# Performance work log

Hardware: AMD Instinct MI355X
Metric: run time of the kernel (lower is better)

## Reference

```python
import jax, jax.numpy as jnp
import numpy as np

DIM = 128


def setup_inputs() -> dict:
    key = jax.random.key(0)
    k1, k2, k3, k4 = jax.random.split(key, 4)
    x = jax.random.normal(k1, (8, 32768, DIM), dtype=jnp.float32)
    # nn.Linear(dim, dim*3, bias=False): weight applied as x @ W.T; store as [dim, 3*dim]
    W_qkv = jax.random.normal(k2, (DIM, 3 * DIM), dtype=jnp.float32) * (DIM ** -0.5)
    W_out = jax.random.normal(k3, (DIM, DIM), dtype=jnp.float32) * (DIM ** -0.5)
    b_out = jax.random.normal(k4, (DIM,), dtype=jnp.float32) * 0.01
    return {"x": x, "W_qkv": W_qkv, "W_out": W_out, "b_out": b_out}


def reference(x, W_qkv, W_out, b_out):
    dim = x.shape[-1]
    scale = dim ** -0.5
    qkv = x @ W_qkv  # [b, n, 3d]
    q, k, v = jnp.split(qkv, 3, axis=-1)
    q = jax.nn.softmax(q, axis=-1) * scale
    k = jax.nn.softmax(k, axis=-1)
    v = jax.nn.softmax(v, axis=-1)
    context = jnp.einsum('bnd,bne->bde', q, k)  # [b, d, d]
    out = jnp.einsum('bde,bne->bnd', context, v)  # [b, n, d]
    return out @ W_out + b_out
```

## Files before the change

### kernel.cpp

```cpp
#include <hip/hip_runtime.h>

#define SEQ 32768
#define QSCALE 0.08838834764831845f
#define NCH 16

typedef __attribute__((ext_vector_type(8))) short short8;
typedef __attribute__((ext_vector_type(8))) __bf16 bf16x8;
typedef __attribute__((ext_vector_type(16))) float f32x16;
typedef __attribute__((ext_vector_type(4))) float f32x4;
typedef __attribute__((ext_vector_type(4))) int int4v;
typedef __attribute__((ext_vector_type(2))) int int2v;

#define SWZ(r, c) ((((r) << 7) + (c)) ^ (((r) & 15) << 3))
#define PSWZ(ch, n) ((((ch) << 6) + (n)) ^ (((ch) & 7) << 3))

__device__ __forceinline__ int cvtpk(float lo, float hi) {
  int r;
  asm("v_cvt_pk_bf16_f32 %0, %1, %2" : "=v"(r) : "v"(lo), "v"(hi));
  return r;
}

__device__ __forceinline__ short bf16b(float f) {
  unsigned u = __builtin_bit_cast(unsigned, f);
  u += 0x7fffu + ((u >> 16) & 1u);
  return (short)(u >> 16);
}

__device__ __forceinline__ f32x16 mfma_ii(int4v a, int4v b, f32x16 c) {
  return __builtin_amdgcn_mfma_f32_32x32x16_bf16(
      __builtin_bit_cast(bf16x8, a), __builtin_bit_cast(bf16x8, b), c, 0, 0, 0);
}

__device__ __forceinline__ int4v build_frag(float e0, float e1, float e2, float e3,
                                            float e4, float e5, float e6, float e7,
                                            int hi) {
  int t0 = cvtpk(e0, e1), t1 = cvtpk(e2, e3);
  int t2 = cvtpk(e4, e5), t3 = cvtpk(e6, e7);
  const int u0 = __shfl_xor(t2, 32), u1 = __shfl_xor(t3, 32);
  const int u2 = __shfl_xor(t0, 32), u3 = __shfl_xor(t1, 32);
  int4v f;
  f[0] = hi ? u0 : t0;
  f[1] = hi ? u1 : t1;
  f[2] = hi ? t2 : u2;
  f[3] = hi ? t3 : u3;
  return f;
}

__global__ void la_prep(const float* __restrict__ Wqkv, int4v* __restrict__ Wf) {
  const int fid = blockIdx.x * 256 + threadIdx.x;
  if (fid >= 6144) return;
  const int side = fid >> 11;
  const int rem = fid & 2047;
  const int tile = rem >> 9;
  const int ks = (rem >> 6) & 7;
  const int lane = rem & 63;
  const int k0 = ks * 16 + ((lane >> 5) << 3);
  const int col = side * 128 + tile * 32 + (lane & 31);
  int4v f;
  #pragma unroll
  for (int a = 0; a < 4; ++a)
    f[a] = cvtpk(Wqkv[(k0 + 2 * a) * 384 + col], Wqkv[(k0 + 2 * a + 1) * 384 + col]);
  Wf[fid] = f;
}

__global__ __launch_bounds__(1024, 4)
void la_pass1(const float* __restrict__ x, const int4v* __restrict__ Wf,
              float* __restrict__ partials) {
  __shared__ __align__(16) short xs[2][64 * 128];
  __shared__ __align__(16) short ptile[2][2][128 * 64];
  __shared__ __align__(16) float sumbuf[2][2][2][32][4];

  const int tid = threadIdx.x;
  const int lane = tid & 63;
  const int wv = tid >> 6;
  const int l31 = lane & 31;
  const int hi = lane >> 5;
  const int koff = hi << 3;
  const int h = wv >> 3;
  const int c = (wv >> 1) & 3;
  const int rh = wv & 1;
  const int td = wv >> 2;
  const int te = wv & 3;
  const int b = blockIdx.x >> 5;
  const int strip = blockIdx.x & 31;
  const long base = (long)b * SEQ + (long)strip * (NCH * 64);

  int4v wf[8];
  #pragma unroll
  for (int ks = 0; ks < 8; ++ks)
    wf[ks] = Wf[((((h << 2) + c) << 3) + ks) * 64 + lane];

  const int lr = tid >> 4;
  const int cf = (tid & 15) << 3;
  {
    const float* xp = x + (base + lr) * 128 + cf;
    f32x4 u0 = *(const f32x4*)xp;
    f32x4 u1 = *(const f32x4*)(xp + 4);
    int4v p;
    p[0] = cvtpk(u0[0], u0[1]); p[1] = cvtpk(u0[2], u0[3]);
    p[2] = cvtpk(u1[0], u1[1]); p[3] = cvtpk(u1[2], u1[3]);
    *(int4v*)&xs[0][SWZ(lr, cf)] = p;
  }
  __syncthreads();

  f32x16 ctx = {0.f};
  const int r0 = rh << 5;
  for (int i = 0; i < NCH; ++i) {
    const int cur = i & 1;
    const int inx = (i + 1 < NCH) ? i + 1 : i;
    const float* xp = x + (base + inx * 64 + lr) * 128 + cf;
    f32x4 u0 = *(const f32x4*)xp;
    f32x4 u1 = *(const f32x4*)(xp + 4);

    f32x16 acc = {0.f};
    #pragma unroll
    for (int ks = 0; ks < 8; ++ks) {
      const int4v xf = *(const int4v*)&xs[cur][SWZ(r0 + l31, (ks << 4) + koff)];
      acc = mfma_ii(wf[ks], xf, acc);
    }
    {
      float sa = 0.f, sb = 0.f;
      #pragma unroll
      for (int r = 0; r < 16; r += 2) {
        acc[r] = __expf(acc[r]);     sa += acc[r];
        acc[r + 1] = __expf(acc[r + 1]); sb += acc[r + 1];
      }
      float s = sa + sb;
      s += __shfl_xor(s, 32);
      if (!hi) sumbuf[cur][h][rh][l31][c] = s;
    }

    {
      int4v p;
      p[0] = cvtpk(u0[0], u0[1]); p[1] = cvtpk(u0[2], u0[3]);
      p[2] = cvtpk(u1[0], u1[1]); p[3] = cvtpk(u1[2], u1[3]);
      *(int4v*)&xs[cur ^ 1][SWZ(lr, cf)] = p;
    }
    __syncthreads();

    if (i > 0) {
      const int pb = cur ^ 1;
      #pragma unroll
      for (int ks = 0; ks < 4; ++ks) {
        const int4v aq = *(const int4v*)&ptile[pb][0][PSWZ((td << 5) + l31, (ks << 4) + koff)];
        const int4v bk = *(const int4v*)&ptile[pb][1][PSWZ((te << 5) + l31, (ks << 4) + koff)];
        ctx = mfma_ii(aq, bk, ctx);
      }
    }

    {
      short* pt = &ptile[cur][h][0];
      const int n = (rh << 5) + l31;
      if (h == 0) {
        const f32x4 sq = *(const f32x4*)&sumbuf[cur][0][rh][l31][0];
        const f32x4 sk = *(const f32x4*)&sumbuf[cur][1][rh][l31][0];
        const float invn = QSCALE * __builtin_amdgcn_rcpf(
            (sq[0] + sq[1] + sq[2] + sq[3]) * (sk[0] + sk[1] + sk[2] + sk[3]));
        #pragma unroll
        for (int r = 0; r < 16; ++r) {
          const int ch = (c << 5) + (r & 3) + ((r >> 2) << 3) + (hi << 2);
          pt[PSWZ(ch, n)] = bf16b(acc[r] * invn);
        }
      } else {
        #pragma unroll
        for (int r = 0; r < 16; ++r) {
          const int ch = (c << 5) + (r & 3) + ((r >> 2) << 3) + (hi << 2);
          pt[PSWZ(ch, n)] = bf16b(acc[r]);
        }
      }
    }
  }
  __syncthreads();
  {
    const int pb = (NCH - 1) & 1;
    #pragma unroll
    for (int ks = 0; ks < 4; ++ks) {
      const int4v aq = *(const int4v*)&ptile[pb][0][PSWZ((td << 5) + l31, (ks << 4) + koff)];
      const int4v bk = *(const int4v*)&ptile[pb][1][PSWZ((te << 5) + l31, (ks << 4) + koff)];
      ctx = mfma_ii(aq, bk, ctx);
    }
  }

  float* pout = partials + (long)blockIdx.x * 16384;
  #pragma unroll
  for (int r = 0; r < 16; ++r) {
    const int drow = (td << 5) + (r & 3) + ((r >> 2) << 3) + (hi << 2);
    pout[(drow << 7) + (te << 5) + l31] = ctx[r];
  }
}

__global__ void la_reduce(const float* __restrict__ partials, float* __restrict__ ctx,
                          int strips) {
  const int b = blockIdx.x >> 4;
  const int sl = blockIdx.x & 15;
  const int idx = (sl << 10) + ((int)threadIdx.x << 2);
  f32x4 acc = {0.f};
  for (int st = 0; st < strips; ++st)
    acc += *(const f32x4*)(partials + ((long)(b * strips + st) << 14) + idx);
  *(f32x4*)(ctx + ((long)b << 14) + idx) = acc;
}

__global__ void la_mkern(const float* __restrict__ ctx, const float* __restrict__ Wout,
                         int4v* __restrict__ Mtf) {
  __shared__ __align__(16) float cl[128 * 132];
  __shared__ float wo[128 * 32];
  const int tid = threadIdx.x;
  const int b = blockIdx.x >> 2;
  const int d0 = (blockIdx.x & 3) << 5;
  const float* cp = ctx + ((long)b << 14);
  for (int i = tid << 2; i < 16384; i += 1024) {
    f32x4 v = *(const f32x4*)(cp + i);
    *(f32x4*)&cl[(i >> 7) * 132 + (i & 127)] = v;
  }
  for (int i = tid; i < 128 * 32; i += 256)
    wo[i] = Wout[((i >> 5) << 7) + d0 + (i & 31)];
  __syncthreads();
  const int dq = tid >> 3;
  const int e0 = (tid & 7) << 4;
  float acc[16];
  #pragma unroll
  for (int i = 0; i < 16; ++i) acc[i] = 0.0f;
  for (int d = 0; d < 128; ++d) {
    const float w = wo[(d << 5) + dq];
    const float* cr = &cl[d * 132 + e0];
    #pragma unroll
    for (int i = 0; i < 16; ++i) acc[i] += cr[i] * w;
  }
  const int dp = d0 + dq;
  const int j = dp & 3, l = dp >> 2, ks = e0 >> 4;
  int4v lo, hi2;
  lo[0] = cvtpk(acc[0], acc[1]);   lo[1] = cvtpk(acc[2], acc[3]);
  lo[2] = cvtpk(acc[4], acc[5]);   lo[3] = cvtpk(acc[6], acc[7]);
  hi2[0] = cvtpk(acc[8], acc[9]);  hi2[1] = cvtpk(acc[10], acc[11]);
  hi2[2] = cvtpk(acc[12], acc[13]); hi2[3] = cvtpk(acc[14], acc[15]);
  int4v* dst = Mtf + ((((long)b << 2) + j) * 8 + ks) * 64;
  dst[l] = lo;
  dst[32 + l] = hi2;
}

__global__ __launch_bounds__(256, 3)
void la_pass2(const float* __restrict__ x, const int4v* __restrict__ Wf,
              const int4v* __restrict__ Mtf, const float* __restrict__ bout,
              float* __restrict__ out) {
  __shared__ __align__(16) short xs[4][32 * 128];

  const int tid = threadIdx.x;
  const int lane = tid & 63;
  const int wv = tid >> 6;
  const int l31 = lane & 31;
  const int hi = lane >> 5;
  const int koff = hi << 3;
  const int b = blockIdx.x >> 8;
  const int chunk = blockIdx.x & 255;
  const long row0 = (long)b * SEQ + (long)chunk * 128 + (wv << 5);

  {
    const float* xb = x + row0 * 128;
    f32x4 u[16];
    #pragma unroll
    for (int t = 0; t < 16; ++t)
      u[t] = *(const f32x4*)(xb + t * 256 + lane * 4);
    #pragma unroll
    for (int t = 0; t < 16; ++t) {
      const int flat = t * 256 + lane * 4;
      int2v w;
      w[0] = cvtpk(u[t][0], u[t][1]);
      w[1] = cvtpk(u[t][2], u[t][3]);
      *(int2v*)&xs[wv][SWZ(flat >> 7, flat & 127)] = w;
    }
  }
  const f32x4 bias = *(const f32x4*)(bout + (l31 << 2));
  asm volatile("s_waitcnt lgkmcnt(0)" ::: "memory");
  __builtin_amdgcn_sched_barrier(0);

  int4v xfr[8];
  #pragma unroll
  for (int ks = 0; ks < 8; ++ks)
    xfr[ks] = *(const int4v*)&xs[wv][SWZ(l31, (ks << 4) + koff)];

  const int4v* WvT = Wf + 2 * 2048;
  f32x16 a0 = {0.f}, a1 = {0.f}, a2 = {0.f}, a3 = {0.f};
  #pragma unroll
  for (int ks = 0; ks < 8; ++ks) {
    a0 = mfma_ii(WvT[(0 * 8 + ks) * 64 + lane], xfr[ks], a0);
    a1 = mfma_ii(WvT[(1 * 8 + ks) * 64 + lane], xfr[ks], a1);
    a2 = mfma_ii(WvT[(2 * 8 + ks) * 64 + lane], xfr[ks], a2);
    a3 = mfma_ii(WvT[(3 * 8 + ks) * 64 + lane], xfr[ks], a3);
  }

  float s = 0.f;
  #pragma unroll
  for (int r = 0; r < 16; ++r) {
    a0[r] = __expf(a0[r]); s += a0[r];
    a1[r] = __expf(a1[r]); s += a1[r];
    a2[r] = __expf(a2[r]); s += a2[r];
    a3[r] = __expf(a3[r]); s += a3[r];
  }
  s += __shfl_xor(s, 32);
  const float inv = __builtin_amdgcn_rcpf(s);
  #pragma unroll
  for (int r = 0; r < 16; ++r) {
    a0[r] *= inv; a1[r] *= inv; a2[r] *= inv; a3[r] *= inv;
  }

  int4v vf[8];
  vf[0] = build_frag(a0[0], a0[1], a0[2], a0[3], a0[4], a0[5], a0[6], a0[7], hi);
  vf[1] = build_frag(a0[8], a0[9], a0[10], a0[11], a0[12], a0[13], a0[14], a0[15], hi);
  vf[2] = build_frag(a1[0], a1[1], a1[2], a1[3], a1[4], a1[5], a1[6], a1[7], hi);
  vf[3] = build_frag(a1[8], a1[9], a1[10], a1[11], a1[12], a1[13], a1[14], a1[15], hi);
  vf[4] = build_frag(a2[0], a2[1], a2[2], a2[3], a2[4], a2[5], a2[6], a2[7], hi);
  vf[5] = build_frag(a2[8], a2[9], a2[10], a2[11], a2[12], a2[13], a2[14], a2[15], hi);
  vf[6] = build_frag(a3[0], a3[1], a3[2], a3[3], a3[4], a3[5], a3[6], a3[7], hi);
  vf[7] = build_frag(a3[8], a3[9], a3[10], a3[11], a3[12], a3[13], a3[14], a3[15], hi);

  const int4v* MtB = Mtf + ((long)b << 11);
  f32x16 o0 = {0.f}, o1 = {0.f}, o2 = {0.f}, o3 = {0.f};
  #pragma unroll
  for (int ks = 0; ks < 8; ++ks) {
    o0 = mfma_ii(vf[ks], MtB[(0 * 8 + ks) * 64 + lane], o0);
    o1 = mfma_ii(vf[ks], MtB[(1 * 8 + ks) * 64 + lane], o1);
    o2 = mfma_ii(vf[ks], MtB[(2 * 8 + ks) * 64 + lane], o2);
    o3 = mfma_ii(vf[ks], MtB[(3 * 8 + ks) * 64 + lane], o3);
  }

  float* obase = out + row0 * 128 + (l31 << 2);
  #pragma unroll
  for (int r = 0; r < 16; ++r) {
    const int n = (r & 3) + ((r >> 2) << 3) + (hi << 2);
    f32x4 v;
    v[0] = o0[r] + bias[0];
    v[1] = o1[r] + bias[1];
    v[2] = o2[r] + bias[2];
    v[3] = o3[r] + bias[3];
    *(f32x4*)(obase + (long)n * 128) = v;
  }
}

extern "C" void kernel_launch(void* const* d_in, const int* in_sizes, int n_in,
                              void* d_out, int out_size, void* d_ws, size_t ws_size,
                              hipStream_t stream) {
  const float* x = (const float*)d_in[0];
  const float* Wqkv = (const float*)d_in[1];
  const float* Wout = (const float*)d_in[2];
  const float* bout = (const float*)d_in[3];
  float* out = (float*)d_out;

  const int strips = 32;

  float* partials = (float*)d_ws;
  float* ctx = partials + (size_t)8 * strips * 16384;
  int4v* Mtf = (int4v*)(ctx + 8 * 16384);
  int4v* Wf = Mtf + 16384;

  la_prep<<<dim3(24), dim3(256), 0, stream>>>(Wqkv, Wf);
  la_pass1<<<dim3(8 * strips), dim3(1024), 0, stream>>>(x, Wf, partials);
  la_reduce<<<dim3(128), dim3(256), 0, stream>>>(partials, ctx, strips);
  la_mkern<<<dim3(32), dim3(256), 0, stream>>>(ctx, Wout, Mtf);
  la_pass2<<<dim3(2048), dim3(256), 0, stream>>>(x, Wf, Mtf, bout, out);
}
```

Before: 149.3 us.

## Double strips in pass1 when workspace allows and single-buffer probability tiles

Makes the strip count and chunks-per-strip runtime parameters. It launches 64 strips per batch (512 blocks) instead of 32 when the workspace is large enough, to give more parallelism across CUs. It also drops the double buffering of ptile and sumbuf and adds a barrier per chunk, so the context MFMA now runs right after the tiles are written instead of overlapping with the next chunk. This frees LDS but adds serialization inside each iteration, and doubles the partials the reduce kernel has to read.

```diff
diff --git a/kernel.cpp b/kernel.cpp
--- a/kernel.cpp
+++ b/kernel.cpp
@@ -2,7 +2,6 @@
 
 #define SEQ 32768
 #define QSCALE 0.08838834764831845f
-#define NCH 16
 
 typedef __attribute__((ext_vector_type(8))) short short8;
 typedef __attribute__((ext_vector_type(8))) __bf16 bf16x8;
@@ -65,10 +64,10 @@
 
 __global__ __launch_bounds__(1024, 4)
 void la_pass1(const float* __restrict__ x, const int4v* __restrict__ Wf,
-              float* __restrict__ partials) {
+              float* __restrict__ partials, int strips, int nch) {
   __shared__ __align__(16) short xs[2][64 * 128];
-  __shared__ __align__(16) short ptile[2][2][128 * 64];
-  __shared__ __align__(16) float sumbuf[2][2][2][32][4];
+  __shared__ __align__(16) short ptile[2][128 * 64];
+  __shared__ __align__(16) float sumbuf[2][2][32][4];
 
   const int tid = threadIdx.x;
   const int lane = tid & 63;
@@ -81,9 +80,9 @@
   const int rh = wv & 1;
   const int td = wv >> 2;
   const int te = wv & 3;
-  const int b = blockIdx.x >> 5;
-  const int strip = blockIdx.x & 31;
-  const long base = (long)b * SEQ + (long)strip * (NCH * 64);
+  const int b = blockIdx.x / strips;
+  const int strip = blockIdx.x - b * strips;
+  const long base = (long)b * SEQ + (long)strip * (nch * 64);
 
   int4v wf[8];
   #pragma unroll
@@ -105,9 +104,9 @@
 
   f32x16 ctx = {0.f};
   const int r0 = rh << 5;
-  for (int i = 0; i < NCH; ++i) {
+  for (int i = 0; i < nch; ++i) {
     const int cur = i & 1;
-    const int inx = (i + 1 < NCH) ? i + 1 : i;
+    const int inx = (i + 1 < nch) ? i + 1 : i;
     const float* xp = x + (base + inx * 64 + lr) * 128 + cf;
     f32x4 u0 = *(const f32x4*)xp;
     f32x4 u1 = *(const f32x4*)(xp + 4);
@@ -122,12 +121,12 @@
       float sa = 0.f, sb = 0.f;
       #pragma unroll
       for (int r = 0; r < 16; r += 2) {
-        acc[r] = __expf(acc[r]);     sa += acc[r];
+        acc[r] = __expf(acc[r]);         sa += acc[r];
         acc[r + 1] = __expf(acc[r + 1]); sb += acc[r + 1];
       }
       float s = sa + sb;
       s += __shfl_xor(s, 32);
-      if (!hi) sumbuf[cur][h][rh][l31][c] = s;
+      if (!hi) sumbuf[h][rh][l31][c] = s;
     }
 
     {
@@ -138,22 +137,12 @@
     }
     __syncthreads();
 
-    if (i > 0) {
-      const int pb = cur ^ 1;
-      #pragma unroll
-      for (int ks = 0; ks < 4; ++ks) {
-        const int4v aq = *(const int4v*)&ptile[pb][0][PSWZ((td << 5) + l31, (ks << 4) + koff)];
-        const int4v bk = *(const int4v*)&ptile[pb][1][PSWZ((te << 5) + l31, (ks << 4) + koff)];
-        ctx = mfma_ii(aq, bk, ctx);
-      }
-    }
-
     {
-      short* pt = &ptile[cur][h][0];
+      short* pt = &ptile[h][0];
       const int n = (rh << 5) + l31;
       if (h == 0) {
-        const f32x4 sq = *(const f32x4*)&sumbuf[cur][0][rh][l31][0];
-        const f32x4 sk = *(const f32x4*)&sumbuf[cur][1][rh][l31][0];
+        const f32x4 sq = *(const f32x4*)&sumbuf[0][rh][l31][0];
+        const f32x4 sk = *(const f32x4*)&sumbuf[1][rh][l31][0];
         const float invn = QSCALE * __builtin_amdgcn_rcpf(
             (sq[0] + sq[1] + sq[2] + sq[3]) * (sk[0] + sk[1] + sk[2] + sk[3]));
         #pragma unroll
@@ -169,14 +158,12 @@
         }
       }
     }
-  }
-  __syncthreads();
-  {
-    const int pb = (NCH - 1) & 1;
+    __syncthreads();
+
     #pragma unroll
     for (int ks = 0; ks < 4; ++ks) {
-      const int4v aq = *(const int4v*)&ptile[pb][0][PSWZ((td << 5) + l31, (ks << 4) + koff)];
-      const int4v bk = *(const int4v*)&ptile[pb][1][PSWZ((te << 5) + l31, (ks << 4) + koff)];
+      const int4v aq = *(const int4v*)&ptile[0][PSWZ((td << 5) + l31, (ks << 4) + koff)];
+      const int4v bk = *(const int4v*)&ptile[1][PSWZ((te << 5) + l31, (ks << 4) + koff)];
       ctx = mfma_ii(aq, bk, ctx);
     }
   }
@@ -345,7 +332,9 @@
   const float* bout = (const float*)d_in[3];
   float* out = (float*)d_out;
 
-  const int strips = 32;
+  const size_t fixed = (size_t)8 * 16384 * 4 + (size_t)16384 * 16 + (size_t)6144 * 16;
+  const int strips = (ws_size >= (size_t)8 * 64 * 16384 * 4 + fixed) ? 64 : 32;
+  const int nch = SEQ / (strips * 64);
 
   float* partials = (float*)d_ws;
   float* ctx = partials + (size_t)8 * strips * 16384;
@@ -353,7 +342,7 @@
   int4v* Wf = Mtf + 16384;
 
   la_prep<<<dim3(24), dim3(256), 0, stream>>>(Wqkv, Wf);
-  la_pass1<<<dim3(8 * strips), dim3(1024), 0, stream>>>(x, Wf, partials);
+  la_pass1<<<dim3(8 * strips), dim3(1024), 0, stream>>>(x, Wf, partials, strips, nch);
   la_reduce<<<dim3(128), dim3(256), 0, stream>>>(partials, ctx, strips);
   la_mkern<<<dim3(32), dim3(256), 0, stream>>>(ctx, Wout, Mtf);
   la_pass2<<<dim3(2048), dim3(256), 0, stream>>>(x, Wf, Mtf, bout, out);
```

Measured after the change: 166.7 us. +11.6%, slower.
